# Kernel tuning notes

Hardware: AMD Instinct MI355X
Metric: run time of the kernel (lower is better)

## Reference

```python
import jax, jax.numpy as jnp
import numpy as np

B, H, S, D = 4, 16, 2048, 128


def setup_inputs() -> dict:
    key = jax.random.key(0)
    kq, kk, kv = jax.random.split(key, 3)
    query = jax.random.normal(kq, (B, H, S, D), dtype=jnp.float32)
    key_t = jax.random.normal(kk, (B, H, S, D), dtype=jnp.float32)
    value = jax.random.normal(kv, (B, H, S, D), dtype=jnp.float32)
    # causal mask, broadcast over batch and heads: True = keep
    mask = jnp.tril(jnp.ones((S, S), dtype=bool))[None, None].repeat(B, 0).repeat(H, 1)
    return {"query": query, "key": key_t, "value": value, "mask": mask}


def reference(query, key, value, mask):
    scale = 1.0 / np.sqrt(D).astype(np.float32)
    # [b,h,sq,sk] scores
    scores = jnp.einsum("bhqd,bhkd->bhqk", query, key) * scale
    scores = jnp.where(mask, scores, -jnp.inf)
    probs = jax.nn.softmax(scores, axis=-1)
    return jnp.einsum("bhqk,bhkd->bhqd", probs, value)
```

## Files before the change

### kernel.cpp

```cpp
#include <hip/hip_runtime.h>


#define SLEN 2048
#define DDIM 128
#define NBH  64
#define QB   256
#define KB   64
#define NITEMS 512

typedef __bf16 bf16x8 __attribute__((ext_vector_type(8)));
typedef float  f32x16 __attribute__((ext_vector_type(16)));
typedef float  f32x4  __attribute__((ext_vector_type(4)));
typedef unsigned uint32x4 __attribute__((ext_vector_type(4)));
typedef unsigned short ushort_t;
typedef ushort_t ushort8 __attribute__((ext_vector_type(8)));

__device__ inline ushort_t f2bf(float f) {
  union { float f; unsigned u; } v; v.f = f;
  unsigned u = v.u;
  u += 0x7FFFu + ((u >> 16) & 1u);
  return (ushort_t)(u >> 16);
}

__device__ inline unsigned cvtpk_bf16(float lo, float hi) {
  unsigned r;
  asm("v_cvt_pk_bf16_f32 %0, %1, %2" : "=v"(r) : "v"(lo), "v"(hi));
  return r;
}

__device__ inline float exp2_fast(float x) {
  float r;
  asm("v_exp_f32 %0, %1" : "=v"(r) : "v"(x));
  return r;
}

__global__ __launch_bounds__(256) void prepass_kernel(
    const float* __restrict__ K, const float* __restrict__ V,
    ushort_t* __restrict__ Kb, ushort_t* __restrict__ Vt,
    int* __restrict__ cnt) {
  __shared__ float t[64][33];
  if (blockIdx.x == 0 && threadIdx.x == 0) *cnt = 0;
  if (blockIdx.x < 2048) {
    const int n4 = (int)((size_t)NBH * SLEN * DDIM / 4);
    const int stride = 2048 * 256;
    for (int i = blockIdx.x * 256 + threadIdx.x; i < n4; i += stride) {
      float4 x = reinterpret_cast<const float4*>(K)[i];
      unsigned lo = (unsigned)f2bf(x.x) | ((unsigned)f2bf(x.y) << 16);
      unsigned hi = (unsigned)f2bf(x.z) | ((unsigned)f2bf(x.w) << 16);
      reinterpret_cast<uint2*>(Kb)[i] = make_uint2(lo, hi);
    }
  } else {
    const int vb = (int)blockIdx.x - 2048;
    const int bh = vb >> 7;
    const int d0 = ((vb >> 5) & 3) * 32;
    const int s0 = (vb & 31) * 64;
    const int tx = threadIdx.x & 31;
    const int ty = threadIdx.x >> 5;
    const float* src = V + ((size_t)bh * SLEN + s0) * DDIM + d0;
#pragma unroll
    for (int j = 0; j < 8; ++j) {
      int sl = ty + j * 8;
      t[sl][tx] = src[(size_t)sl * DDIM + tx];
    }
    __syncthreads();
    ushort_t* dst = Vt + ((size_t)bh * DDIM + d0) * SLEN + s0;
#pragma unroll
    for (int j = 0; j < 4; ++j) {
      int dl = ty + j * 8;
      unsigned lo = f2bf(t[tx * 2][dl]);
      unsigned hi = f2bf(t[tx * 2 + 1][dl]);
      *reinterpret_cast<unsigned*>(&dst[(size_t)dl * SLEN + tx * 2]) =
          lo | (hi << 16);
    }
  }
}

__global__ __launch_bounds__(512, 2) void fattn8_kernel(
    const float* __restrict__ Q, const ushort_t* __restrict__ Kb,
    const ushort_t* __restrict__ Vt, float* __restrict__ Out,
    int* __restrict__ cnt) {
  __shared__ ushort_t K_sh[2][KB * DDIM];
  __shared__ ushort_t V_sh[2][DDIM * KB];
  __shared__ int item_sh;

  const int tid  = threadIdx.x;
  const int lane = tid & 63;
  const int wv   = tid >> 6;
  const int l31  = lane & 31;
  const int hi   = lane >> 5;

  const float qscale = 0.12751744f;
  const float THR = 11.0f;

  while (true) {
    if (tid == 0) item_sh = atomicAdd(cnt, 1);
    __syncthreads();
    const int item = item_sh;
    if (item >= NITEMS) break;

    const int qblk = 7 - (item >> 6);
    const int bh   = item & 63;

    const float*    Qp = Q  + (size_t)bh * SLEN * DDIM;
    const ushort_t* Kp = Kb + (size_t)bh * SLEN * DDIM;
    const ushort_t* Vp = Vt + (size_t)bh * DDIM * SLEN;
    float*          Op = Out + (size_t)bh * SLEN * DDIM;

    const int q0w = qblk * QB + wv * 32;
    const int qg  = q0w + l31;

    bf16x8 qf[8];
    {
      const float* qr = Qp + (size_t)qg * DDIM;
#pragma unroll
      for (int ds = 0; ds < 8; ++ds) {
        int d0 = ds * 16 + hi * 8;
        float4 x = *reinterpret_cast<const float4*>(qr + d0);
        float4 y = *reinterpret_cast<const float4*>(qr + d0 + 4);
        ushort8 uu;
        uu[0] = f2bf(x.x * qscale); uu[1] = f2bf(x.y * qscale);
        uu[2] = f2bf(x.z * qscale); uu[3] = f2bf(x.w * qscale);
        uu[4] = f2bf(y.x * qscale); uu[5] = f2bf(y.y * qscale);
        uu[6] = f2bf(y.z * qscale); uu[7] = f2bf(y.w * qscale);
        qf[ds] = __builtin_bit_cast(bf16x8, uu);
      }
    }

    f32x16 Oacc[4];
#pragma unroll
    for (int dt = 0; dt < 4; ++dt)
#pragma unroll
      for (int r = 0; r < 16; ++r) Oacc[dt][r] = 0.f;
    float m_run = -3.0e38f, l_run = 0.f;

    const int last_kb       = qblk * 4 + 3;
    const int last_kb_wave  = (q0w + 31) >> 6;

    auto stage = [&](int buf, int kb) {
      const ushort_t* ksrc = Kp + (size_t)kb * KB * DDIM;
#pragma unroll
      for (int j = 0; j < 2; ++j) {
        int chunk = wv * 128 + j * 64 + lane;
        int row = chunk >> 4, c = chunk & 15;
        const ushort_t* g = ksrc + row * DDIM + ((c ^ (row & 7)) << 3);
        ushort_t* l = &K_sh[buf][(wv * 128 + j * 64) * 8];
        __builtin_amdgcn_global_load_lds(
            (const __attribute__((address_space(1))) unsigned*)g,
            (__attribute__((address_space(3))) unsigned*)l, 16, 0, 0);
      }
      const ushort_t* vsrc = Vp + (size_t)kb * KB;
#pragma unroll
      for (int j = 0; j < 2; ++j) {
        int chunk = wv * 128 + j * 64 + lane;
        int row = chunk >> 3, c = chunk & 7;
        const ushort_t* g = vsrc + (size_t)row * SLEN + ((c ^ (row & 7)) << 3);
        ushort_t* l = &V_sh[buf][(wv * 128 + j * 64) * 8];
        __builtin_amdgcn_global_load_lds(
            (const __attribute__((address_space(1))) unsigned*)g,
            (__attribute__((address_space(3))) unsigned*)l, 16, 0, 0);
      }
    };

    stage(0, 0);

    for (int kb = 0; kb <= last_kb; ++kb) {
      __syncthreads();
      if (kb < last_kb) stage((kb + 1) & 1, kb + 1);

      if (kb <= last_kb_wave) {
        const int buf = kb & 1;

        f32x16 sac[2];
#pragma unroll
        for (int mt = 0; mt < 2; ++mt) {
          f32x16 a;
#pragma unroll
          for (int r = 0; r < 16; ++r) a[r] = 0.f;
          int row = mt * 32 + l31;
          int sw = row & 7;
          __builtin_amdgcn_s_setprio(1);
#pragma unroll
          for (int ds = 0; ds < 8; ++ds) {
            int c = ds * 2 + hi;
            bf16x8 kf = *reinterpret_cast<const bf16x8*>(
                &K_sh[buf][row * DDIM + ((c ^ sw) << 3)]);
            a = __builtin_amdgcn_mfma_f32_32x32x16_bf16(kf, qf[ds], a, 0, 0, 0);
          }
          __builtin_amdgcn_s_setprio(0);
          sac[mt] = a;
        }

        if (kb * 64 + 63 > q0w) {
#pragma unroll
          for (int mt = 0; mt < 2; ++mt) {
            int kbase = kb * 64 + mt * 32 + 4 * hi;
#pragma unroll
            for (int r = 0; r < 16; ++r) {
              int krow = (r & 3) + 8 * (r >> 2);
              if (kbase + krow > qg) sac[mt][r] = -3.0e38f;
            }
          }
        }

        float p0 = sac[0][0], p1 = sac[0][1], p2 = sac[0][2], p3 = sac[0][3];
#pragma unroll
        for (int r = 4; r < 16; r += 4) {
          p0 = fmaxf(p0, sac[0][r + 0]); p1 = fmaxf(p1, sac[0][r + 1]);
          p2 = fmaxf(p2, sac[0][r + 2]); p3 = fmaxf(p3, sac[0][r + 3]);
        }
#pragma unroll
        for (int r = 0; r < 16; r += 4) {
          p0 = fmaxf(p0, sac[1][r + 0]); p1 = fmaxf(p1, sac[1][r + 1]);
          p2 = fmaxf(p2, sac[1][r + 2]); p3 = fmaxf(p3, sac[1][r + 3]);
        }
        float tm = fmaxf(fmaxf(p0, p1), fmaxf(p2, p3));
        tm = fmaxf(tm, __shfl_xor(tm, 32));

        if (!__all(tm - m_run <= THR)) {
          float mnew  = fmaxf(m_run, tm);
          float alpha = exp2_fast(m_run - mnew);
          m_run = mnew;
          l_run *= alpha;
#pragma unroll
          for (int dt = 0; dt < 4; ++dt)
#pragma unroll
            for (int r = 0; r < 16; ++r) Oacc[dt][r] *= alpha;
        }

        float s0 = 0.f, s1 = 0.f, s2 = 0.f, s3 = 0.f;
#pragma unroll
        for (int mt = 0; mt < 2; ++mt)
#pragma unroll
          for (int r = 0; r < 16; r += 4) {
            float e0 = exp2_fast(sac[mt][r + 0] - m_run);
            float e1 = exp2_fast(sac[mt][r + 1] - m_run);
            float e2 = exp2_fast(sac[mt][r + 2] - m_run);
            float e3 = exp2_fast(sac[mt][r + 3] - m_run);
            sac[mt][r + 0] = e0; sac[mt][r + 1] = e1;
            sac[mt][r + 2] = e2; sac[mt][r + 3] = e3;
            s0 += e0; s1 += e1; s2 += e2; s3 += e3;
          }
        float rs = (s0 + s1) + (s2 + s3);
        rs += __shfl_xor(rs, 32);
        l_run += rs;

        uint32x4 pw[4];
#pragma unroll
        for (int ks = 0; ks < 4; ++ks) {
          const int mt = ks >> 1;
          const int hb = 8 * (ks & 1);
          unsigned X  = cvtpk_bf16(sac[mt][hb + 0], sac[mt][hb + 1]);
          unsigned X2 = cvtpk_bf16(sac[mt][hb + 2], sac[mt][hb + 3]);
          unsigned Y  = cvtpk_bf16(sac[mt][hb + 4], sac[mt][hb + 5]);
          unsigned Y2 = cvtpk_bf16(sac[mt][hb + 6], sac[mt][hb + 7]);
          asm("v_permlane32_swap_b32 %0, %1" : "+v"(X),  "+v"(Y));
          asm("v_permlane32_swap_b32 %0, %1" : "+v"(X2), "+v"(Y2));
          uint32x4 f; f.x = X; f.y = X2; f.z = Y; f.w = Y2;
          pw[ks] = f;
        }

#pragma unroll
        for (int dt = 0; dt < 4; ++dt) {
          int row = dt * 32 + l31;
          int sw = row & 7;
          __builtin_amdgcn_s_setprio(1);
#pragma unroll
          for (int ks = 0; ks < 4; ++ks) {
            int c = ks * 2 + hi;
            bf16x8 vf = *reinterpret_cast<const bf16x8*>(
                &V_sh[buf][row * 64 + ((c ^ sw) << 3)]);
            Oacc[dt] = __builtin_amdgcn_mfma_f32_32x32x16_bf16(
                vf, __builtin_bit_cast(bf16x8, pw[ks]), Oacc[dt], 0, 0, 0);
          }
          __builtin_amdgcn_s_setprio(0);
        }
      }
    }

    {
      float invl = 1.0f / l_run;
      float* orow = Op + (size_t)qg * DDIM;
#pragma unroll
      for (int dt = 0; dt < 4; ++dt)
#pragma unroll
        for (int rq = 0; rq < 4; ++rq) {
          float4 o;
          o.x = Oacc[dt][rq * 4 + 0] * invl;
          o.y = Oacc[dt][rq * 4 + 1] * invl;
          o.z = Oacc[dt][rq * 4 + 2] * invl;
          o.w = Oacc[dt][rq * 4 + 3] * invl;
          int d = dt * 32 + 8 * rq + 4 * hi;
          *reinterpret_cast<float4*>(orow + d) = o;
        }
    }
    __syncthreads();
  }
}

__global__ __launch_bounds__(256) void fattn_kernel(
    const float* __restrict__ Q, const float* __restrict__ K,
    const float* __restrict__ V, float* __restrict__ Out) {
  __shared__ ushort_t Kf_sh[64 * 128];
  __shared__ ushort_t Vf_sh[128 * 64];
  __shared__ ushort_t P_sh[4][16 * 64];

  const int tid  = threadIdx.x;
  const int lane = tid & 63;
  const int wv   = tid >> 6;
  const int l16  = lane & 15;
  const int lhi  = lane >> 4;
  const int qblk = blockIdx.x;
  const int bh   = blockIdx.y;
  const float scale = 0.08838834764831845f;

  const size_t base = (size_t)bh * SLEN * DDIM;
  const float* Qp = Q + base;
  const float* Kp = K + base;
  const float* Vp = V + base;
  float*       Op = Out + base;

  bf16x8 qf[4];
  {
    const int qrow = qblk * 64 + wv * 16 + l16;
    const float* qr = Qp + (size_t)qrow * DDIM;
#pragma unroll
    for (int dc = 0; dc < 4; ++dc) {
      int d0 = dc * 32 + lhi * 8;
      float4 x = *reinterpret_cast<const float4*>(qr + d0);
      float4 y = *reinterpret_cast<const float4*>(qr + d0 + 4);
      ushort8 uu;
      uu[0] = f2bf(x.x * scale); uu[1] = f2bf(x.y * scale);
      uu[2] = f2bf(x.z * scale); uu[3] = f2bf(x.w * scale);
      uu[4] = f2bf(y.x * scale); uu[5] = f2bf(y.y * scale);
      uu[6] = f2bf(y.z * scale); uu[7] = f2bf(y.w * scale);
      qf[dc] = __builtin_bit_cast(bf16x8, uu);
    }
  }

  f32x4 Oacc[8];
#pragma unroll
  for (int i = 0; i < 8; ++i) Oacc[i] = (f32x4){0.f, 0.f, 0.f, 0.f};
  float m_run[4], l_run[4];
#pragma unroll
  for (int r = 0; r < 4; ++r) { m_run[r] = -3.0e38f; l_run[r] = 0.f; }

  for (int kb = 0; kb <= qblk; ++kb) {
    __syncthreads();
    {
      const float* src = Kp + (size_t)kb * 64 * DDIM;
#pragma unroll
      for (int it = 0; it < 8; ++it) {
        int idx4 = it * 256 + tid;
        int r  = idx4 >> 5;
        int c4 = idx4 & 31;
        float4 x = *reinterpret_cast<const float4*>(src + r * DDIM + c4 * 4);
        unsigned lo = ((unsigned)f2bf(x.y) << 16) | f2bf(x.x);
        unsigned hh = ((unsigned)f2bf(x.w) << 16) | f2bf(x.z);
        int e = (r * 128 + c4 * 4) ^ ((r & 7) << 3);
        *reinterpret_cast<uint2*>(&Kf_sh[e]) = make_uint2(lo, hh);
      }
      const float* vs = Vp + (size_t)kb * 64 * DDIM;
#pragma unroll
      for (int it = 0; it < 8; ++it) {
        int idx4 = it * 256 + tid;
        int r  = idx4 >> 5;
        int c4 = idx4 & 31;
        float4 x = *reinterpret_cast<const float4*>(vs + r * DDIM + c4 * 4);
        int c0 = c4 * 4;
        float vals[4] = {x.x, x.y, x.z, x.w};
#pragma unroll
        for (int j = 0; j < 4; ++j) {
          int d = c0 + j;
          Vf_sh[(d * 64 + r) ^ ((d & 7) << 3)] = f2bf(vals[j]);
        }
      }
    }
    __syncthreads();

    f32x4 sacc[4];
#pragma unroll
    for (int g = 0; g < 4; ++g) {
      f32x4 acc = (f32x4){0.f, 0.f, 0.f, 0.f};
#pragma unroll
      for (int dc = 0; dc < 4; ++dc) {
        int row = g * 16 + l16;
        int e = (row * 128 + dc * 32 + lhi * 8) ^ ((row & 7) << 3);
        bf16x8 kf = *reinterpret_cast<const bf16x8*>(&Kf_sh[e]);
        acc = __builtin_amdgcn_mfma_f32_16x16x32_bf16(qf[dc], kf, acc, 0, 0, 0);
      }
      sacc[g] = acc;
    }

    if (kb == qblk) {
      int q0 = lhi * 4;
#pragma unroll
      for (int g = 0; g < 4; ++g) {
        int kcol = g * 16 + l16;
#pragma unroll
        for (int r = 0; r < 4; ++r) {
          if (kcol > wv * 16 + q0 + r) sacc[g][r] = -3.0e38f;
        }
      }
    }

    float tmax[4];
#pragma unroll
    for (int r = 0; r < 4; ++r)
      tmax[r] = fmaxf(fmaxf(sacc[0][r], sacc[1][r]),
                      fmaxf(sacc[2][r], sacc[3][r]));
#pragma unroll
    for (int x = 1; x < 16; x <<= 1) {
#pragma unroll
      for (int r = 0; r < 4; ++r)
        tmax[r] = fmaxf(tmax[r], __shfl_xor(tmax[r], x));
    }

    float alpha[4], mnew[4];
#pragma unroll
    for (int r = 0; r < 4; ++r) {
      mnew[r]  = fmaxf(m_run[r], tmax[r]);
      alpha[r] = __expf(m_run[r] - mnew[r]);
      m_run[r] = mnew[r];
    }

    float rsum[4] = {0.f, 0.f, 0.f, 0.f};
#pragma unroll
    for (int g = 0; g < 4; ++g) {
#pragma unroll
      for (int r = 0; r < 4; ++r) {
        float p = __expf(sacc[g][r] - mnew[r]);
        rsum[r] += p;
        int prow = lhi * 4 + r;
        P_sh[wv][(prow * 64 + g * 16 + l16) ^ ((prow & 7) << 3)] = f2bf(p);
      }
    }
#pragma unroll
    for (int x = 1; x < 16; x <<= 1) {
#pragma unroll
      for (int r = 0; r < 4; ++r) rsum[r] += __shfl_xor(rsum[r], x);
    }
#pragma unroll
    for (int r = 0; r < 4; ++r) l_run[r] = l_run[r] * alpha[r] + rsum[r];

#pragma unroll
    for (int dg = 0; dg < 8; ++dg)
#pragma unroll
      for (int r = 0; r < 4; ++r) Oacc[dg][r] *= alpha[r];

    bf16x8 pf[2];
#pragma unroll
    for (int kc = 0; kc < 2; ++kc) {
      int e = (l16 * 64 + kc * 32 + lhi * 8) ^ ((l16 & 7) << 3);
      pf[kc] = *reinterpret_cast<const bf16x8*>(&P_sh[wv][e]);
    }
#pragma unroll
    for (int dg = 0; dg < 8; ++dg) {
#pragma unroll
      for (int kc = 0; kc < 2; ++kc) {
        int row = dg * 16 + l16;
        int e = (row * 64 + kc * 32 + lhi * 8) ^ ((row & 7) << 3);
        bf16x8 vf = *reinterpret_cast<const bf16x8*>(&Vf_sh[e]);
        Oacc[dg] = __builtin_amdgcn_mfma_f32_16x16x32_bf16(pf[kc], vf, Oacc[dg], 0, 0, 0);
      }
    }
  }

#pragma unroll
  for (int r = 0; r < 4; ++r) {
    float inv = 1.0f / l_run[r];
    int q = qblk * 64 + wv * 16 + lhi * 4 + r;
    float* orow = Op + (size_t)q * DDIM;
#pragma unroll
    for (int dg = 0; dg < 8; ++dg)
      orow[dg * 16 + l16] = Oacc[dg][r] * inv;
  }
}

extern "C" void kernel_launch(void* const* d_in, const int* in_sizes, int n_in,
                              void* d_out, int out_size, void* d_ws, size_t ws_size,
                              hipStream_t stream) {
  const float* Q = (const float*)d_in[0];
  const float* K = (const float*)d_in[1];
  const float* V = (const float*)d_in[2];
  float* O = (float*)d_out;

  const size_t n_elem = (size_t)NBH * SLEN * DDIM;
  const size_t need   = n_elem * 2 * 2 + 64;

  if (ws_size >= need) {
    ushort_t* Kbf = (ushort_t*)d_ws;
    ushort_t* Vt  = Kbf + n_elem;
    int* cnt      = (int*)(Vt + n_elem);
    prepass_kernel<<<2048 + 8192, 256, 0, stream>>>(K, V, Kbf, Vt, cnt);
    fattn8_kernel<<<dim3(NITEMS), dim3(512), 0, stream>>>(Q, Kbf, Vt, O, cnt);
  } else {
    fattn_kernel<<<dim3(SLEN / 64, NBH), dim3(256), 0, stream>>>(Q, K, V, O);
  }
}
```

Baseline: 142.0 us.

## Fuse K bf16 conversion into attention kernel via register-staged loads

Removes the K fp32-to-bf16 prepass. The attention kernel now loads fp32 K tiles into registers one iteration ahead, converts them with packed bf16 conversion, and writes them swizzled into LDS after the compute, with one barrier per iteration. This saves a full read and write of the bf16 K copy in global memory. In exchange it reads twice as many K bytes inside the main loop, gives up the async global_load_lds path for K, and adds register pressure and conversion ALU work. Because K tiles are reused across query blocks, K is converted several times.

```diff
diff --git a/kernel.cpp b/kernel.cpp
--- a/kernel.cpp
+++ b/kernel.cpp
@@ -35,48 +35,36 @@
 }
 
 __global__ __launch_bounds__(256) void prepass_kernel(
-    const float* __restrict__ K, const float* __restrict__ V,
-    ushort_t* __restrict__ Kb, ushort_t* __restrict__ Vt,
+    const float* __restrict__ V, ushort_t* __restrict__ Vt,
     int* __restrict__ cnt) {
   __shared__ float t[64][33];
   if (blockIdx.x == 0 && threadIdx.x == 0) *cnt = 0;
-  if (blockIdx.x < 2048) {
-    const int n4 = (int)((size_t)NBH * SLEN * DDIM / 4);
-    const int stride = 2048 * 256;
-    for (int i = blockIdx.x * 256 + threadIdx.x; i < n4; i += stride) {
-      float4 x = reinterpret_cast<const float4*>(K)[i];
-      unsigned lo = (unsigned)f2bf(x.x) | ((unsigned)f2bf(x.y) << 16);
-      unsigned hi = (unsigned)f2bf(x.z) | ((unsigned)f2bf(x.w) << 16);
-      reinterpret_cast<uint2*>(Kb)[i] = make_uint2(lo, hi);
-    }
-  } else {
-    const int vb = (int)blockIdx.x - 2048;
-    const int bh = vb >> 7;
-    const int d0 = ((vb >> 5) & 3) * 32;
-    const int s0 = (vb & 31) * 64;
-    const int tx = threadIdx.x & 31;
-    const int ty = threadIdx.x >> 5;
-    const float* src = V + ((size_t)bh * SLEN + s0) * DDIM + d0;
-#pragma unroll
-    for (int j = 0; j < 8; ++j) {
-      int sl = ty + j * 8;
-      t[sl][tx] = src[(size_t)sl * DDIM + tx];
-    }
-    __syncthreads();
-    ushort_t* dst = Vt + ((size_t)bh * DDIM + d0) * SLEN + s0;
-#pragma unroll
-    for (int j = 0; j < 4; ++j) {
-      int dl = ty + j * 8;
-      unsigned lo = f2bf(t[tx * 2][dl]);
-      unsigned hi = f2bf(t[tx * 2 + 1][dl]);
-      *reinterpret_cast<unsigned*>(&dst[(size_t)dl * SLEN + tx * 2]) =
-          lo | (hi << 16);
-    }
-  }
-}
-
-__global__ __launch_bounds__(512, 2) void fattn8_kernel(
-    const float* __restrict__ Q, const ushort_t* __restrict__ Kb,
+  const int vb = (int)blockIdx.x;
+  const int bh = vb >> 7;
+  const int d0 = ((vb >> 5) & 3) * 32;
+  const int s0 = (vb & 31) * 64;
+  const int tx = threadIdx.x & 31;
+  const int ty = threadIdx.x >> 5;
+  const float* src = V + ((size_t)bh * SLEN + s0) * DDIM + d0;
+#pragma unroll
+  for (int j = 0; j < 8; ++j) {
+    int sl = ty + j * 8;
+    t[sl][tx] = src[(size_t)sl * DDIM + tx];
+  }
+  __syncthreads();
+  ushort_t* dst = Vt + ((size_t)bh * DDIM + d0) * SLEN + s0;
+#pragma unroll
+  for (int j = 0; j < 4; ++j) {
+    int dl = ty + j * 8;
+    unsigned lo = f2bf(t[tx * 2][dl]);
+    unsigned hi = f2bf(t[tx * 2 + 1][dl]);
+    *reinterpret_cast<unsigned*>(&dst[(size_t)dl * SLEN + tx * 2]) =
+        lo | (hi << 16);
+  }
+}
+
+__global__ __launch_bounds__(512, 2) void fattn9_kernel(
+    const float* __restrict__ Q, const float* __restrict__ Kf32,
     const ushort_t* __restrict__ Vt, float* __restrict__ Out,
     int* __restrict__ cnt) {
   __shared__ ushort_t K_sh[2][KB * DDIM];
@@ -92,6 +80,14 @@
   const float qscale = 0.12751744f;
   const float THR = 11.0f;
 
+  float4 kr0a, kr0b, kr1a, kr1b;
+  const int kch0 = tid;
+  const int kch1 = 512 + tid;
+  const int krow0 = kch0 >> 4, kp0 = kch0 & 15;
+  const int krow1 = kch1 >> 4, kp1 = kch1 & 15;
+  const int kgc0 = kp0 ^ (krow0 & 7);
+  const int kgc1 = kp1 ^ (krow1 & 7);
+
   while (true) {
     if (tid == 0) item_sh = atomicAdd(cnt, 1);
     __syncthreads();
@@ -101,10 +97,10 @@
     const int qblk = 7 - (item >> 6);
     const int bh   = item & 63;
 
-    const float*    Qp = Q  + (size_t)bh * SLEN * DDIM;
-    const ushort_t* Kp = Kb + (size_t)bh * SLEN * DDIM;
-    const ushort_t* Vp = Vt + (size_t)bh * DDIM * SLEN;
-    float*          Op = Out + (size_t)bh * SLEN * DDIM;
+    const float*    Qp = Q    + (size_t)bh * SLEN * DDIM;
+    const float*    Kp = Kf32 + (size_t)bh * SLEN * DDIM;
+    const ushort_t* Vp = Vt   + (size_t)bh * DDIM * SLEN;
+    float*          Op = Out  + (size_t)bh * SLEN * DDIM;
 
     const int q0w = qblk * QB + wv * 32;
     const int qg  = q0w + l31;
@@ -136,18 +132,25 @@
     const int last_kb       = qblk * 4 + 3;
     const int last_kb_wave  = (q0w + 31) >> 6;
 
-    auto stage = [&](int buf, int kb) {
-      const ushort_t* ksrc = Kp + (size_t)kb * KB * DDIM;
-#pragma unroll
-      for (int j = 0; j < 2; ++j) {
-        int chunk = wv * 128 + j * 64 + lane;
-        int row = chunk >> 4, c = chunk & 15;
-        const ushort_t* g = ksrc + row * DDIM + ((c ^ (row & 7)) << 3);
-        ushort_t* l = &K_sh[buf][(wv * 128 + j * 64) * 8];
-        __builtin_amdgcn_global_load_lds(
-            (const __attribute__((address_space(1))) unsigned*)g,
-            (__attribute__((address_space(3))) unsigned*)l, 16, 0, 0);
-      }
+    auto kload = [&](int kb) {
+      const float* ksrc = Kp + (size_t)kb * KB * DDIM;
+      const float* g0 = ksrc + krow0 * DDIM + kgc0 * 8;
+      const float* g1 = ksrc + krow1 * DDIM + kgc1 * 8;
+      kr0a = *reinterpret_cast<const float4*>(g0);
+      kr0b = *reinterpret_cast<const float4*>(g0 + 4);
+      kr1a = *reinterpret_cast<const float4*>(g1);
+      kr1b = *reinterpret_cast<const float4*>(g1 + 4);
+    };
+    auto kwrite = [&](int buf) {
+      uint32x4 w0, w1;
+      w0.x = cvtpk_bf16(kr0a.x, kr0a.y); w0.y = cvtpk_bf16(kr0a.z, kr0a.w);
+      w0.z = cvtpk_bf16(kr0b.x, kr0b.y); w0.w = cvtpk_bf16(kr0b.z, kr0b.w);
+      w1.x = cvtpk_bf16(kr1a.x, kr1a.y); w1.y = cvtpk_bf16(kr1a.z, kr1a.w);
+      w1.z = cvtpk_bf16(kr1b.x, kr1b.y); w1.w = cvtpk_bf16(kr1b.z, kr1b.w);
+      *reinterpret_cast<uint32x4*>(&K_sh[buf][krow0 * DDIM + kp0 * 8]) = w0;
+      *reinterpret_cast<uint32x4*>(&K_sh[buf][krow1 * DDIM + kp1 * 8]) = w1;
+    };
+    auto vstage = [&](int buf, int kb) {
       const ushort_t* vsrc = Vp + (size_t)kb * KB;
 #pragma unroll
       for (int j = 0; j < 2; ++j) {
@@ -161,15 +164,19 @@
       }
     };
 
-    stage(0, 0);
+    kload(0);
+    vstage(0, 0);
+    kwrite(0);
+    __syncthreads();
 
     for (int kb = 0; kb <= last_kb; ++kb) {
-      __syncthreads();
-      if (kb < last_kb) stage((kb + 1) & 1, kb + 1);
+      const int buf = kb & 1;
+      if (kb < last_kb) {
+        kload(kb + 1);
+        vstage(buf ^ 1, kb + 1);
+      }
 
       if (kb <= last_kb_wave) {
-        const int buf = kb & 1;
-
         f32x16 sac[2];
 #pragma unroll
         for (int mt = 0; mt < 2; ++mt) {
@@ -275,6 +282,9 @@
           __builtin_amdgcn_s_setprio(0);
         }
       }
+
+      if (kb < last_kb) kwrite(buf ^ 1);
+      __syncthreads();
     }
 
     {
@@ -485,14 +495,13 @@
   float* O = (float*)d_out;
 
   const size_t n_elem = (size_t)NBH * SLEN * DDIM;
-  const size_t need   = n_elem * 2 * 2 + 64;
+  const size_t need   = n_elem * 2 + 64;
 
   if (ws_size >= need) {
-    ushort_t* Kbf = (ushort_t*)d_ws;
-    ushort_t* Vt  = Kbf + n_elem;
-    int* cnt      = (int*)(Vt + n_elem);
-    prepass_kernel<<<2048 + 8192, 256, 0, stream>>>(K, V, Kbf, Vt, cnt);
-    fattn8_kernel<<<dim3(NITEMS), dim3(512), 0, stream>>>(Q, Kbf, Vt, O, cnt);
+    ushort_t* Vt = (ushort_t*)d_ws;
+    int* cnt     = (int*)(Vt + n_elem);
+    prepass_kernel<<<8192, 256, 0, stream>>>(V, Vt, cnt);
+    fattn9_kernel<<<dim3(NITEMS), dim3(512), 0, stream>>>(Q, K, Vt, O, cnt);
   } else {
     fattn_kernel<<<dim3(SLEN / 64, NBH), dim3(256), 0, stream>>>(Q, K, V, O);
   }
```

Result: faster. 136.5 us (median of 3 runs) (-3.9%).
